# Optimization experiments

Hardware: AMD Instinct MI355X
Metric: run time of the kernel (lower is better)

## Reference

```python
import jax, jax.numpy as jnp
import numpy as np

L, B, S, D = 8, 1, 4096, 2048
H, KVH, HD = 16, 2, 128
Q = 32
THETA = 1e6
MROPE = (16, 24, 24)  # mrope_section, sums to HD//2
EPS = 1e-6


def setup_inputs() -> dict:
    key = jax.random.key(0)
    ks = jax.random.split(key, 8)
    hidden_states = jax.random.normal(ks[0], (L, B, S, D), dtype=jnp.float32)
    ln_w = jax.random.uniform(ks[1], (L, D), dtype=jnp.float32, minval=0.5, maxval=1.5)
    q_w = jax.random.normal(ks[2], (L, D, H * HD), dtype=jnp.float32) * 0.02
    q_b = jax.random.normal(ks[3], (L, H * HD), dtype=jnp.float32) * 0.02
    k_w = jax.random.normal(ks[4], (L, D, KVH * HD), dtype=jnp.float32) * 0.02
    k_b = jax.random.normal(ks[5], (L, KVH * HD), dtype=jnp.float32) * 0.02
    position_ids = jax.random.randint(ks[6], (3, B, S), 0, S, dtype=jnp.int32)
    q_idx = jnp.sort(jax.random.randint(ks[7], (Q,), 0, S, dtype=jnp.int32))
    return {"hidden_states": hidden_states, "ln_w": ln_w, "q_w": q_w, "q_b": q_b,
            "k_w": k_w, "k_b": k_b, "position_ids": position_ids, "q_idx": q_idx}


def _rot_half(x):
    h = x.shape[-1] // 2
    return jnp.concatenate([-x[..., h:], x[..., :h]], axis=-1)


def _mrope_combine(t):
    # t: (3, B, S, HD). Split last dim per 2*mrope_section, chunk i taken from axis i%3.
    parts, off = [], 0
    for i, sec in enumerate(MROPE):
        w = 2 * sec
        parts.append(t[i % 3, :, :, off:off + w])
        off += w
    return jnp.concatenate(parts, axis=-1)[:, None, :, :]  # (B, 1, S, HD)


def reference(hidden_states, ln_w, q_w, q_b, k_w, k_b, position_ids, q_idx):
    # Rotary embeddings from 3D mRoPE position ids
    inv_freq = 1.0 / (THETA ** (jnp.arange(0, HD, 2, dtype=jnp.float32) / HD))  # (HD/2,)
    freqs = position_ids.astype(jnp.float32)[..., None] * inv_freq  # (3, B, S, HD/2)
    emb = jnp.concatenate([freqs, freqs], axis=-1)  # (3, B, S, HD)
    cos = _mrope_combine(jnp.cos(emb))  # (B, 1, S, HD)
    sin = _mrope_combine(jnp.sin(emb))
    cos_q = cos[:, :, q_idx, :]  # (B, 1, Q, HD)
    sin_q = sin[:, :, q_idx, :]
    # Eager causal mask sliced at query rows: (Q, S)
    mask_add = jnp.where(jnp.arange(S)[None, :] > q_idx[:, None], -1e9, 0.0).astype(jnp.float32)

    scale = 1.0 / np.sqrt(HD).astype(np.float32)

    def per_layer(hs, lw, qw, qb, kw, kb):
        # RMSNorm (input_layernorm)
        var = jnp.mean(jnp.square(hs), axis=-1, keepdims=True)
        x = hs * jax.lax.rsqrt(var + EPS) * lw  # (B, S, D)
        xq = x[:, q_idx, :]  # (B, Q, D)
        k = (jnp.einsum('bsd,de->bse', x, kw) + kb).reshape(B, S, KVH, HD).transpose(0, 2, 1, 3)
        q = (jnp.einsum('bqd,de->bqe', xq, qw) + qb).reshape(B, Q, H, HD).transpose(0, 2, 1, 3)
        k = jnp.repeat(k, H // KVH, axis=1)  # repeat_kv -> (B, H, S, HD)
        k = k * cos + _rot_half(k) * sin
        q = q * cos_q + _rot_half(q) * sin_q
        scores = jnp.einsum('bhqd,bhkd->bhqk', q, k) * scale  # (B, H, Q, S)
        scores = scores + mask_add[None, None]
        return jax.nn.softmax(scores.astype(jnp.float32), axis=-1)

    return jax.vmap(per_layer)(hidden_states, ln_w, q_w, q_b, k_w, k_b)  # (L, B, H, Q, S)
```

## Files before the change

### kernel.cpp

```cpp
#include <hip/hip_runtime.h>
#include <hip/hip_bf16.h>
#include <math.h>

#define LYR 8
#define SEQ 4096
#define DIM 2048
#define NH 16
#define HD 128
#define NQ 32
#define NKV 256
#define NQE 2048

typedef __attribute__((ext_vector_type(8))) short short8;
typedef __attribute__((ext_vector_type(4))) float f32x4;

#define WS_IRQ   0
#define WS_ABLOB 256
#define WS_COS   524544
#define WS_SIN   1048832
#define WS_QBUF  1573120
#define WS_PART  2097408
#define WS_W2    4194560
#define WS_KBLOB 8388864
#define WS_QBLOB 16777472

__device__ __forceinline__ short f2bf(float x) {
  __hip_bfloat16 h = __float2bfloat16(x);
  return *(short*)&h;
}
__device__ __forceinline__ float bf2f(short s) {
  unsigned u = ((unsigned)(unsigned short)s) << 16;
  return __uint_as_float(u);
}

#define GLOAD16(srcp, dstp) \
  __builtin_amdgcn_global_load_lds( \
      (const __attribute__((address_space(1))) unsigned int*)(srcp), \
      (__attribute__((address_space(3))) unsigned int*)(dstp), 16, 0, 0)

#define RBAR() asm volatile("s_waitcnt lgkmcnt(0)\n\ts_barrier" ::: "memory")

__global__ __launch_bounds__(256) void prep_kernel(
    const float* __restrict__ ln_w, const float* __restrict__ k_w,
    short* __restrict__ W2) {
  int kb = blockIdx.x, l = blockIdx.y, t = threadIdx.x;
  const float* kwl = k_w + (size_t)l * DIM * NKV;
  const float* lnl = ln_w + l * DIM;
  short* blob = W2 + (size_t)(l * 64 + kb) * 16384;
  #pragma unroll
  for (int i = 0; i < 4; ++i) {
    int p = t + i * 256;
    int fi = p >> 6, lane = p & 63;
    int n = fi * 16 + (lane & 15);
    int k0 = kb * 32 + (lane >> 4) * 8;
    short hi8[8], lo8[8];
    #pragma unroll
    for (int e = 0; e < 8; ++e) {
      float v = lnl[k0 + e] * kwl[(size_t)(k0 + e) * NKV + n];
      short h = f2bf(v);
      hi8[e] = h;
      lo8[e] = f2bf(v - bf2f(h));
    }
    *(short8*)(blob + p * 8) = *(short8*)hi8;
    *(short8*)(blob + 8192 + p * 8) = *(short8*)lo8;
  }
}

__global__ __launch_bounds__(256) void rmsq_kernel(const float* __restrict__ hs,
                                                   const int* __restrict__ q_idx,
                                                   float* __restrict__ irq) {
  int qi = blockIdx.x, l = blockIdx.y, t = threadIdx.x;
  int s = q_idx[qi];
  const float* row = hs + ((size_t)l * SEQ + s) * DIM;
  float4 v0 = *(const float4*)(row + t * 4);
  float4 v1 = *(const float4*)(row + t * 4 + 1024);
  float acc = v0.x*v0.x + v0.y*v0.y + v0.z*v0.z + v0.w*v0.w
            + v1.x*v1.x + v1.y*v1.y + v1.z*v1.z + v1.w*v1.w;
  #pragma unroll
  for (int off = 32; off >= 1; off >>= 1) acc += __shfl_down(acc, off);
  __shared__ float red[4];
  if ((t & 63) == 0) red[t >> 6] = acc;
  __syncthreads();
  if (t == 0) {
    float tot = red[0] + red[1] + red[2] + red[3];
    irq[l * NQ + qi] = rsqrtf(tot / (float)DIM + 1e-6f);
  }
}

__global__ void cossin_kernel(const int* __restrict__ pos_ids,
                              float* __restrict__ cost, float* __restrict__ sint) {
  int idx = blockIdx.x * 256 + threadIdx.x;
  int s = idx >> 7, d = idx & 127;
  int t = (d < 32) ? 0 : (d < 80 ? 1 : 2);
  int j = d & 63;
  double invf = pow(1000000.0, -(double)j / 64.0);
  double ph = (double)pos_ids[t * SEQ + s] * invf;
  cost[idx] = (float)cos(ph);
  sint[idx] = (float)sin(ph);
}

__global__ __launch_bounds__(256) void xqt_kernel(
    const float* __restrict__ hs, const float* __restrict__ ln_w,
    const int* __restrict__ q_idx, const float* __restrict__ irq,
    short* __restrict__ Ablob) {
  __shared__ int qix[32];
  __shared__ float qir[32];
  int l = blockIdx.x, t = threadIdx.x;
  if (t < 32) { qix[t] = q_idx[t]; qir[t] = irq[l * NQ + t]; }
  __syncthreads();
  int lane = t & 63, g4 = t >> 6;
  short* base = Ablob + (size_t)l * 131072;
  int row = lane & 15, kgl = lane >> 4;
  for (int i = 0; i < 64; ++i) {
    int group = g4 * 64 + i;
    int kb = group >> 2, half = (group >> 1) & 1, mf = group & 1;
    int r = row + mf * 16;
    int k0 = kb * 32 + kgl * 8;
    const float* src = hs + ((size_t)l * SEQ + qix[r]) * DIM + k0;
    const float* lnp = ln_w + l * DIM + k0;
    float ir = qir[r];
    float4 v0 = *(const float4*)src;
    float4 v1 = *(const float4*)(src + 4);
    float4 w0 = *(const float4*)lnp;
    float4 w1 = *(const float4*)(lnp + 4);
    float av[8] = {v0.x*w0.x, v0.y*w0.y, v0.z*w0.z, v0.w*w0.w,
                   v1.x*w1.x, v1.y*w1.y, v1.z*w1.z, v1.w*w1.w};
    short o8[8];
    #pragma unroll
    for (int e = 0; e < 8; ++e) {
      float v = av[e] * ir;
      short h = f2bf(v);
      o8[e] = half ? f2bf(v - bf2f(h)) : h;
    }
    *(short8*)(base + group * 512 + lane * 8) = *(short8*)o8;
  }
}

__global__ __launch_bounds__(256) void kgemm_kernel(
    const float* __restrict__ hs, const short* __restrict__ W2,
    const float* __restrict__ k_b, const float* __restrict__ cost,
    const float* __restrict__ sint, short* __restrict__ Kblob) {
  __shared__ __align__(1024) char SM[67072];

  int t = threadIdx.x;
  int fid = blockIdx.x;
  int l = fid & 7, sb = fid >> 3;
  int s0 = sb * 64;
  int lane = t & 63, w = t >> 6;
  int fr = lane & 15, kg = lane >> 4;
  int arow = t >> 2, akg = t & 3;

  const float* hrow = hs + ((size_t)l * SEQ + s0 + arow) * DIM + akg * 8;
  const char* wbase = (const char*)(W2 + (size_t)l * 64 * 16384);
  const char* wfrag = wbase + w * 1024 + lane * 16;

  int amf = arow >> 4;
  int awoff = amf * 1024 + (((akg * 16 + (arow & 15)) * 16) ^ (akg << 5));
  int aroff = (lane * 16) ^ ((lane >> 4) << 5);

  f32x4 acc[4][4];
  #pragma unroll
  for (int mf = 0; mf < 4; ++mf)
    #pragma unroll
    for (int nf = 0; nf < 4; ++nf) acc[mf][nf] = (f32x4){0.f, 0.f, 0.f, 0.f};
  float sq = 0.f;
  float4 rA0, rA1, rB0, rB1;
  short8 B0h[4], B0l[4], B1h[4], B1l[4];

  {
    #pragma unroll
    for (int nf = 0; nf < 4; ++nf) {
      B0h[nf] = *(const short8*)(wfrag + nf * 4096);
      B0l[nf] = *(const short8*)(wfrag + nf * 4096 + 16384);
    }
    float4 a0 = *(const float4*)(hrow);
    float4 a1 = *(const float4*)(hrow + 4);
    float av[8] = {a0.x, a0.y, a0.z, a0.w, a1.x, a1.y, a1.z, a1.w};
    short hi8[8], lo8[8];
    #pragma unroll
    for (int e = 0; e < 8; ++e) {
      sq += av[e] * av[e];
      short h = f2bf(av[e]);
      hi8[e] = h;
      lo8[e] = f2bf(av[e] - bf2f(h));
    }
    *(short8*)(SM + awoff) = *(short8*)hi8;
    *(short8*)(SM + 4096 + awoff) = *(short8*)lo8;
    rA0 = *(const float4*)(hrow + 32);
    rA1 = *(const float4*)(hrow + 36);
  }
  RBAR();

#define KSTEP(KB, CA0, CA1, NA0, NA1, UBH, UBL, PBH, PBL) do { \
    int buf_ = (KB) & 1; \
    char* asb_ = SM + buf_ * 8192; \
    if ((KB) < 63) { \
      const char* bsrc_ = wfrag + (size_t)((KB) + 1) * 32768; \
      _Pragma("unroll") \
      for (int nf = 0; nf < 4; ++nf) { \
        PBH[nf] = *(const short8*)(bsrc_ + nf * 4096); \
        PBL[nf] = *(const short8*)(bsrc_ + nf * 4096 + 16384); \
      } \
    } \
    if ((KB) < 62) { \
      NA0 = *(const float4*)(hrow + ((KB) + 2) * 32); \
      NA1 = *(const float4*)(hrow + ((KB) + 2) * 32 + 4); \
    } \
    short8 ah_[4], al_[4]; \
    _Pragma("unroll") \
    for (int mf = 0; mf < 4; ++mf) { \
      ah_[mf] = *(const short8*)(asb_ + mf * 1024 + aroff); \
      al_[mf] = *(const short8*)(asb_ + 4096 + mf * 1024 + aroff); \
    } \
    __builtin_amdgcn_s_setprio(1); \
    _Pragma("unroll") \
    for (int nf = 0; nf < 4; ++nf) { \
      _Pragma("unroll") \
      for (int mf = 0; mf < 4; ++mf) { \
        acc[mf][nf] = __builtin_amdgcn_mfma_f32_16x16x32_bf16(ah_[mf], UBH[nf], acc[mf][nf], 0, 0, 0); \
        acc[mf][nf] = __builtin_amdgcn_mfma_f32_16x16x32_bf16(ah_[mf], UBL[nf], acc[mf][nf], 0, 0, 0); \
        acc[mf][nf] = __builtin_amdgcn_mfma_f32_16x16x32_bf16(al_[mf], UBH[nf], acc[mf][nf], 0, 0, 0); \
      } \
    } \
    __builtin_amdgcn_s_setprio(0); \
    if ((KB) < 63) { \
      char* asn_ = SM + (buf_ ^ 1) * 8192; \
      float av_[8] = {CA0.x, CA0.y, CA0.z, CA0.w, CA1.x, CA1.y, CA1.z, CA1.w}; \
      short hi8_[8], lo8_[8]; \
      _Pragma("unroll") \
      for (int e = 0; e < 8; ++e) { \
        sq += av_[e] * av_[e]; \
        short h_ = f2bf(av_[e]); \
        hi8_[e] = h_; \
        lo8_[e] = f2bf(av_[e] - bf2f(h_)); \
      } \
      *(short8*)(asn_ + awoff) = *(short8*)hi8_; \
      *(short8*)(asn_ + 4096 + awoff) = *(short8*)lo8_; \
    } \
    RBAR(); \
  } while (0)

  for (int kb2 = 0; kb2 < 32; ++kb2) {
    KSTEP(2 * kb2,     rA0, rA1, rB0, rB1, B0h, B0l, B1h, B1l);
    KSTEP(2 * kb2 + 1, rB0, rB1, rA0, rA1, B1h, B1l, B0h, B0l);
  }
#undef KSTEP

  sq += __shfl_xor(sq, 1);
  sq += __shfl_xor(sq, 2);
  float* irs = (float*)(SM + 66560);
  if ((t & 3) == 0) irs[arow] = rsqrtf(sq / (float)DIM + 1e-6f);
  __syncthreads();

  float* Kraw = (float*)SM;
  int j = w * 16 + fr;
  float bias0 = k_b[l * NKV + j];
  float bias1 = k_b[l * NKV + j + 64];
  float bias2 = k_b[l * NKV + j + 128];
  float bias3 = k_b[l * NKV + j + 192];
  #pragma unroll
  for (int mf = 0; mf < 4; ++mf) {
    #pragma unroll
    for (int r = 0; r < 4; ++r) {
      int row = mf * 16 + kg * 4 + r;
      int s = s0 + row;
      float ir = irs[row];
      float v0 = acc[mf][0][r] * ir + bias0;
      float v1 = acc[mf][1][r] * ir + bias1;
      float v2 = acc[mf][2][r] * ir + bias2;
      float v3 = acc[mf][3][r] * ir + bias3;
      float cj = cost[s * HD + j], sj = sint[s * HD + j];
      float cj2 = cost[s * HD + j + 64], sj2 = sint[s * HD + j + 64];
      float* kr = Kraw + row * 260;
      kr[j]       = v0 * cj - v1 * sj;
      kr[j + 64]  = v1 * cj2 + v0 * sj2;
      kr[j + 128] = v2 * cj - v3 * sj;
      kr[j + 192] = v3 * cj2 + v2 * sj2;
    }
  }
  __syncthreads();

  int kc = sb >> 1, fb = (sb & 1) * 4;
  #pragma unroll
  for (int i = 0; i < 8; ++i) {
    int c = t + i * 256;
    int lc = c & 63, fl = (c >> 6) & 3, ts = (c >> 8) & 3, kv = c >> 10;
    int key = fl * 16 + (lc & 15);
    int d0 = kv * 128 + ts * 32 + (lc >> 4) * 8;
    float4 x0 = *(const float4*)(Kraw + key * 260 + d0);
    float4 x1 = *(const float4*)(Kraw + key * 260 + d0 + 4);
    float av[8] = {x0.x, x0.y, x0.z, x0.w, x1.x, x1.y, x1.z, x1.w};
    short hi8[8], lo8[8];
    #pragma unroll
    for (int e = 0; e < 8; ++e) {
      short h = f2bf(av[e]);
      hi8[e] = h;
      lo8[e] = f2bf(av[e] - bf2f(h));
    }
    short* bb = Kblob + (size_t)((l * 2 + kv) * 32 + kc) * 32768
              + (size_t)((ts * 2 + 0) * 8 + fb + fl) * 512 + lc * 8;
    *(short8*)bb = *(short8*)hi8;
    *(short8*)(bb + 4096) = *(short8*)lo8;
  }
}

__global__ __launch_bounds__(512) void qgemm_kernel(
    const float* __restrict__ q_w, const short* __restrict__ Ablob,
    float* __restrict__ part) {
  __shared__ __align__(1024) char SM[131072];
  int t = threadIdx.x;
  int nc = blockIdx.x, ks = blockIdx.y, l = blockIdx.z;
  int lane = t & 63, w = t >> 6;
  int fr = lane & 15, kg = lane >> 4;
  const char* abase = (const char*)(Ablob + (size_t)l * 131072 + (size_t)ks * 32768);
  const float* qwl = q_w + (size_t)l * DIM * NQE;

  #pragma unroll
  for (int c = 0; c < 8; ++c) {
    int chunk = w * 8 + c;
    GLOAD16(abase + chunk * 1024 + lane * 16, SM + chunk * 1024);
  }
  #pragma unroll
  for (int c = 0; c < 4; ++c) {
    int r = w * 4 + c;
    GLOAD16((const char*)(qwl + (size_t)(ks * 512 + r) * NQE + nc * 256) + lane * 16,
            SM + 65536 + r * 1024 + lane * 16);
  }
  f32x4 acc[2][2];
  #pragma unroll
  for (int mf = 0; mf < 2; ++mf)
    #pragma unroll
    for (int nf = 0; nf < 2; ++nf) acc[mf][nf] = (f32x4){0.f, 0.f, 0.f, 0.f};
  __syncthreads();

  for (int ts = 0; ts < 16; ++ts) {
    int buf = ts & 1;
    if (ts < 15) {
      #pragma unroll
      for (int c = 0; c < 4; ++c) {
        int r = w * 4 + c;
        GLOAD16((const char*)(qwl + (size_t)(ks * 512 + (ts + 1) * 32 + r) * NQE + nc * 256) + lane * 16,
                SM + 65536 + (buf ^ 1) * 32768 + r * 1024 + lane * 16);
      }
    }
    short8 ah[2], al[2];
    #pragma unroll
    for (int mf = 0; mf < 2; ++mf) {
      ah[mf] = *(const short8*)(SM + ts * 4096 + mf * 1024 + lane * 16);
      al[mf] = *(const short8*)(SM + ts * 4096 + 2048 + mf * 1024 + lane * 16);
    }
    const float* bt = (const float*)(SM + 65536 + buf * 32768);
    #pragma unroll
    for (int nf = 0; nf < 2; ++nf) {
      int c = w * 32 + nf * 16 + fr;
      short bh8[8], bl8[8];
      #pragma unroll
      for (int e = 0; e < 8; ++e) {
        float v = bt[(kg * 8 + e) * 256 + c];
        short h = f2bf(v);
        bh8[e] = h;
        bl8[e] = f2bf(v - bf2f(h));
      }
      short8 bh = *(short8*)bh8, bl = *(short8*)bl8;
      #pragma unroll
      for (int mf = 0; mf < 2; ++mf) {
        acc[mf][nf] = __builtin_amdgcn_mfma_f32_16x16x32_bf16(ah[mf], bh, acc[mf][nf], 0, 0, 0);
        acc[mf][nf] = __builtin_amdgcn_mfma_f32_16x16x32_bf16(ah[mf], bl, acc[mf][nf], 0, 0, 0);
        acc[mf][nf] = __builtin_amdgcn_mfma_f32_16x16x32_bf16(al[mf], bh, acc[mf][nf], 0, 0, 0);
      }
    }
    __syncthreads();
  }

  #pragma unroll
  for (int mf = 0; mf < 2; ++mf) {
    #pragma unroll
    for (int r = 0; r < 4; ++r) {
      int row = mf * 16 + kg * 4 + r;
      float* prow = part + ((size_t)((ks * LYR + l) * NQ + row)) * NQE + nc * 256;
      #pragma unroll
      for (int nf = 0; nf < 2; ++nf) {
        int col = w * 32 + nf * 16 + fr;
        prow[col] = acc[mf][nf][r];
      }
    }
  }
}

__global__ __launch_bounds__(256) void qred_kernel(
    const float* __restrict__ part, const float* __restrict__ q_b,
    float* __restrict__ Qbuf) {
  int idx = blockIdx.x * 256 + threadIdx.x;
  int n = idx & 2047, q = (idx >> 11) & 31, l = idx >> 16;
  float v = q_b[l * NQE + n];
  #pragma unroll
  for (int ks = 0; ks < 4; ++ks)
    v += part[((size_t)((ks * LYR + l) * NQ + q)) * NQE + n];
  Qbuf[((size_t)l * NQ + q) * NQE + n] = v;
}

__global__ __launch_bounds__(256) void qpack_kernel(
    const float* __restrict__ Qbuf, const float* __restrict__ cost,
    const float* __restrict__ sint, const int* __restrict__ q_idx,
    short* __restrict__ Qblob) {
  int kv = blockIdx.x, l = blockIdx.y, t = threadIdx.x;
  short* blob = Qblob + (size_t)(l * 2 + kv) * 65536;
  #pragma unroll
  for (int i = 0; i < 16; ++i) {
    int p = t + i * 256;
    int ts = p >> 10, f = (p >> 6) & 15, lane = p & 63;
    int row = f * 16 + (lane & 15);
    int hh = row >> 5, q = row & 31;
    int h = kv * 8 + hh;
    int d0 = ts * 32 + (lane >> 4) * 8;
    int s = q_idx[q];
    const float* qrow = Qbuf + ((size_t)l * NQ + q) * NQE + h * HD;
    const float* ct = cost + s * HD;
    const float* st = sint + s * HD;
    short hi8[8], lo8[8];
    #pragma unroll
    for (int e = 0; e < 8; ++e) {
      int d = d0 + e;
      float x = qrow[d];
      float xp = qrow[d ^ 64];
      float v = (d < 64) ? (x * ct[d] - xp * st[d]) : (x * ct[d] + xp * st[d]);
      short h2 = f2bf(v);
      hi8[e] = h2;
      lo8[e] = f2bf(v - bf2f(h2));
    }
    *(short8*)(blob + ((ts * 2 + 0) * 16 + f) * 512 + lane * 8) = *(short8*)hi8;
    *(short8*)(blob + ((ts * 2 + 1) * 16 + f) * 512 + lane * 8) = *(short8*)lo8;
  }
}

__global__ __launch_bounds__(512) void scores_kernel(
    const short* __restrict__ Qblob, const short* __restrict__ Kblob,
    const int* __restrict__ q_idx, float* __restrict__ out) {
  __shared__ short Qs[2][16384];
  __shared__ short Ks[2][8192];
  __shared__ int qiv[32];
  int t = threadIdx.x;
  int kc = blockIdx.x, kv = blockIdx.y, l = blockIdx.z;
  int lane = t & 63, w = t >> 6;
  int wm = w >> 1, wn = w & 1;
  if (t < 32) qiv[t] = q_idx[t];
  const char* qsrc = (const char*)(Qblob + (size_t)(l * 2 + kv) * 65536);
  const char* ksrc = (const char*)(Kblob + (size_t)((l * 2 + kv) * 32 + kc) * 32768);
  #pragma unroll
  for (int c = 0; c < 4; ++c) {
    int off = (w * 4 + c) * 1024;
    GLOAD16(qsrc + off + lane * 16, (char*)Qs[0] + off);
  }
  #pragma unroll
  for (int c = 0; c < 2; ++c) {
    int off = (w * 2 + c) * 1024;
    GLOAD16(ksrc + off + lane * 16, (char*)Ks[0] + off);
  }
  f32x4 acc[4][4];
  #pragma unroll
  for (int mf = 0; mf < 4; ++mf)
    #pragma unroll
    for (int nf = 0; nf < 4; ++nf) acc[mf][nf] = (f32x4){0.f, 0.f, 0.f, 0.f};
  __syncthreads();
  for (int ts = 0; ts < 4; ++ts) {
    int buf = ts & 1;
    if (ts < 3) {
      const char* qs = qsrc + (ts + 1) * 32768;
      const char* ks = ksrc + (ts + 1) * 16384;
      #pragma unroll
      for (int c = 0; c < 4; ++c) {
        int off = (w * 4 + c) * 1024;
        GLOAD16(qs + off + lane * 16, (char*)Qs[(ts + 1) & 1] + off);
      }
      #pragma unroll
      for (int c = 0; c < 2; ++c) {
        int off = (w * 2 + c) * 1024;
        GLOAD16(ks + off + lane * 16, (char*)Ks[(ts + 1) & 1] + off);
      }
    }
    short8 ah[4], al[4];
    #pragma unroll
    for (int mf = 0; mf < 4; ++mf) {
      int f = wm * 4 + mf;
      ah[mf] = *(const short8*)(Qs[buf] + f * 512 + lane * 8);
      al[mf] = *(const short8*)(Qs[buf] + 8192 + f * 512 + lane * 8);
    }
    #pragma unroll
    for (int nf = 0; nf < 4; ++nf) {
      int f = wn * 4 + nf;
      short8 bh = *(const short8*)(Ks[buf] + f * 512 + lane * 8);
      short8 bl = *(const short8*)(Ks[buf] + 4096 + f * 512 + lane * 8);
      #pragma unroll
      for (int mf = 0; mf < 4; ++mf) {
        acc[mf][nf] = __builtin_amdgcn_mfma_f32_16x16x32_bf16(ah[mf], bh, acc[mf][nf], 0, 0, 0);
        acc[mf][nf] = __builtin_amdgcn_mfma_f32_16x16x32_bf16(ah[mf], bl, acc[mf][nf], 0, 0, 0);
        acc[mf][nf] = __builtin_amdgcn_mfma_f32_16x16x32_bf16(al[mf], bh, acc[mf][nf], 0, 0, 0);
      }
    }
    __syncthreads();
  }
  const float scale = 0.088388347648318447f;
  #pragma unroll
  for (int mf = 0; mf < 4; ++mf) {
    #pragma unroll
    for (int r = 0; r < 4; ++r) {
      int rr = wm * 64 + mf * 16 + (lane >> 4) * 4 + r;
      int hh = rr >> 5, q = rr & 31;
      int qv = qiv[q];
      float* orow = out + (((size_t)(l * NH + kv * 8 + hh)) * NQ + q) * SEQ;
      #pragma unroll
      for (int nf = 0; nf < 4; ++nf) {
        int key = kc * 128 + (wn * 4 + nf) * 16 + (lane & 15);
        orow[key] = (key > qv) ? -1e9f : acc[mf][nf][r] * scale;
      }
    }
  }
}

__global__ __launch_bounds__(256) void softmax_kernel(float* __restrict__ out) {
  size_t row = blockIdx.x;
  float* p = out + row * SEQ;
  int t = threadIdx.x;
  float4 v[4];
  float mx = -1e30f;
  #pragma unroll
  for (int i = 0; i < 4; ++i) {
    v[i] = *(const float4*)(p + t * 4 + i * 1024);
    mx = fmaxf(mx, fmaxf(fmaxf(v[i].x, v[i].y), fmaxf(v[i].z, v[i].w)));
  }
  #pragma unroll
  for (int off = 32; off >= 1; off >>= 1) mx = fmaxf(mx, __shfl_xor(mx, off));
  __shared__ float red[4];
  if ((t & 63) == 0) red[t >> 6] = mx;
  __syncthreads();
  mx = fmaxf(fmaxf(red[0], red[1]), fmaxf(red[2], red[3]));
  __syncthreads();
  float sum = 0.f;
  #pragma unroll
  for (int i = 0; i < 4; ++i) {
    v[i].x = __expf(v[i].x - mx); v[i].y = __expf(v[i].y - mx);
    v[i].z = __expf(v[i].z - mx); v[i].w = __expf(v[i].w - mx);
    sum += v[i].x + v[i].y + v[i].z + v[i].w;
  }
  #pragma unroll
  for (int off = 32; off >= 1; off >>= 1) sum += __shfl_xor(sum, off);
  if ((t & 63) == 0) red[t >> 6] = sum;
  __syncthreads();
  sum = red[0] + red[1] + red[2] + red[3];
  float inv = 1.f / sum;
  #pragma unroll
  for (int i = 0; i < 4; ++i) {
    v[i].x *= inv; v[i].y *= inv; v[i].z *= inv; v[i].w *= inv;
    *(float4*)(p + t * 4 + i * 1024) = v[i];
  }
}

extern "C" void kernel_launch(void* const* d_in, const int* in_sizes, int n_in,
                              void* d_out, int out_size, void* d_ws, size_t ws_size,
                              hipStream_t stream) {
  const float* hs   = (const float*)d_in[0];
  const float* ln_w = (const float*)d_in[1];
  const float* q_w  = (const float*)d_in[2];
  const float* q_b  = (const float*)d_in[3];
  const float* k_w  = (const float*)d_in[4];
  const float* k_b  = (const float*)d_in[5];
  const int* pos    = (const int*)d_in[6];
  const int* qidx   = (const int*)d_in[7];
  float* out = (float*)d_out;
  float* ws = (float*)d_ws;
  float* irq   = ws + WS_IRQ;
  short* Ablob = (short*)(ws + WS_ABLOB);
  float* cost  = ws + WS_COS;
  float* sint  = ws + WS_SIN;
  float* Qbuf  = ws + WS_QBUF;
  float* part  = ws + WS_PART;
  short* W2    = (short*)(ws + WS_W2);
  short* Kblob = (short*)(ws + WS_KBLOB);
  short* Qblob = (short*)(ws + WS_QBLOB);

  prep_kernel<<<dim3(64, LYR), 256, 0, stream>>>(ln_w, k_w, W2);
  rmsq_kernel<<<dim3(NQ, LYR), 256, 0, stream>>>(hs, qidx, irq);
  cossin_kernel<<<(SEQ * HD) / 256, 256, 0, stream>>>(pos, cost, sint);
  xqt_kernel<<<LYR, 256, 0, stream>>>(hs, ln_w, qidx, irq, Ablob);
  kgemm_kernel<<<512, 256, 0, stream>>>(hs, W2, k_b, cost, sint, Kblob);
  qgemm_kernel<<<dim3(8, 4, LYR), 512, 0, stream>>>(q_w, Ablob, part);
  qred_kernel<<<2048, 256, 0, stream>>>(part, q_b, Qbuf);
  qpack_kernel<<<dim3(2, LYR), 256, 0, stream>>>(Qbuf, cost, sint, qidx, Qblob);
  scores_kernel<<<dim3(32, 2, LYR), 512, 0, stream>>>(Qblob, Kblob, qidx, out);
  softmax_kernel<<<LYR * NH * NQ, 256, 0, stream>>>(out);
}
```

Baseline: 279.8 us.

## Split-bf16 via bit truncation, interleave MFMA halves with LDS staging, swizzle K tile

```diff
diff --git a/kernel.cpp b/kernel.cpp
--- a/kernel.cpp
+++ b/kernel.cpp
@@ -31,6 +31,13 @@
 __device__ __forceinline__ float bf2f(short s) {
   unsigned u = ((unsigned)(unsigned short)s) << 16;
   return __uint_as_float(u);
+}
+
+__device__ __forceinline__ void split1(float x, short& h, short& l) {
+  unsigned b = __float_as_uint(x);
+  h = (short)(b >> 16);
+  float lo = x - __uint_as_float(b & 0xffff0000u);
+  l = (short)((__float_as_uint(lo) + 0x8000u) >> 16);
 }
 
 #define GLOAD16(srcp, dstp) \
@@ -129,8 +136,9 @@
     #pragma unroll
     for (int e = 0; e < 8; ++e) {
       float v = av[e] * ir;
-      short h = f2bf(v);
-      o8[e] = half ? f2bf(v - bf2f(h)) : h;
+      short hh, ll;
+      split1(v, hh, ll);
+      o8[e] = half ? ll : hh;
     }
     *(short8*)(base + group * 512 + lane * 8) = *(short8*)o8;
   }
@@ -140,7 +148,7 @@
     const float* __restrict__ hs, const short* __restrict__ W2,
     const float* __restrict__ k_b, const float* __restrict__ cost,
     const float* __restrict__ sint, short* __restrict__ Kblob) {
-  __shared__ __align__(1024) char SM[67072];
+  __shared__ __align__(1024) char SM[65536];
 
   int t = threadIdx.x;
   int fid = blockIdx.x;
@@ -154,8 +162,7 @@
   const char* wbase = (const char*)(W2 + (size_t)l * 64 * 16384);
   const char* wfrag = wbase + w * 1024 + lane * 16;
 
-  int amf = arow >> 4;
-  int awoff = amf * 1024 + (((akg * 16 + (arow & 15)) * 16) ^ (akg << 5));
+  int awoff = (arow >> 4) * 1024 + (((akg * 16 + (arow & 15)) * 16) ^ (akg << 5));
   int aroff = (lane * 16) ^ ((lane >> 4) << 5);
 
   f32x4 acc[4][4];
@@ -179,10 +186,8 @@
     short hi8[8], lo8[8];
     #pragma unroll
     for (int e = 0; e < 8; ++e) {
-      sq += av[e] * av[e];
-      short h = f2bf(av[e]);
-      hi8[e] = h;
-      lo8[e] = f2bf(av[e] - bf2f(h));
+      sq = fmaf(av[e], av[e], sq);
+      split1(av[e], hi8[e], lo8[e]);
     }
     *(short8*)(SM + awoff) = *(short8*)hi8;
     *(short8*)(SM + 4096 + awoff) = *(short8*)lo8;
@@ -191,9 +196,10 @@
   }
   RBAR();
 
-#define KSTEP(KB, CA0, CA1, NA0, NA1, UBH, UBL, PBH, PBL) do { \
+#define KSTEP8(KB, CA0, CA1, NA0, NA1, UBH, UBL, PBH, PBL) do { \
     int buf_ = (KB) & 1; \
-    char* asb_ = SM + buf_ * 8192; \
+    const char* asb_ = SM + buf_ * 8192; \
+     \
     if ((KB) < 63) { \
       const char* bsrc_ = wfrag + (size_t)((KB) + 1) * 32768; \
       _Pragma("unroll") \
@@ -212,47 +218,81 @@
       ah_[mf] = *(const short8*)(asb_ + mf * 1024 + aroff); \
       al_[mf] = *(const short8*)(asb_ + 4096 + mf * 1024 + aroff); \
     } \
+    __builtin_amdgcn_s_barrier(); \
+    asm volatile("s_waitcnt lgkmcnt(0)" ::: "memory"); \
     __builtin_amdgcn_s_setprio(1); \
     _Pragma("unroll") \
-    for (int nf = 0; nf < 4; ++nf) { \
-      _Pragma("unroll") \
-      for (int mf = 0; mf < 4; ++mf) { \
+    for (int nf = 0; nf < 2; ++nf) \
+      _Pragma("unroll") \
+      for (int mf = 0; mf < 4; ++mf) \
         acc[mf][nf] = __builtin_amdgcn_mfma_f32_16x16x32_bf16(ah_[mf], UBH[nf], acc[mf][nf], 0, 0, 0); \
+    _Pragma("unroll") \
+    for (int nf = 0; nf < 2; ++nf) \
+      _Pragma("unroll") \
+      for (int mf = 0; mf < 4; ++mf) \
         acc[mf][nf] = __builtin_amdgcn_mfma_f32_16x16x32_bf16(ah_[mf], UBL[nf], acc[mf][nf], 0, 0, 0); \
+    _Pragma("unroll") \
+    for (int nf = 0; nf < 2; ++nf) \
+      _Pragma("unroll") \
+      for (int mf = 0; mf < 4; ++mf) \
         acc[mf][nf] = __builtin_amdgcn_mfma_f32_16x16x32_bf16(al_[mf], UBH[nf], acc[mf][nf], 0, 0, 0); \
-      } \
-    } \
     __builtin_amdgcn_s_setprio(0); \
+    __builtin_amdgcn_s_barrier(); \
+     \
     if ((KB) < 63) { \
       char* asn_ = SM + (buf_ ^ 1) * 8192; \
       float av_[8] = {CA0.x, CA0.y, CA0.z, CA0.w, CA1.x, CA1.y, CA1.z, CA1.w}; \
       short hi8_[8], lo8_[8]; \
       _Pragma("unroll") \
       for (int e = 0; e < 8; ++e) { \
-        sq += av_[e] * av_[e]; \
-        short h_ = f2bf(av_[e]); \
-        hi8_[e] = h_; \
-        lo8_[e] = f2bf(av_[e] - bf2f(h_)); \
+        sq = fmaf(av_[e], av_[e], sq); \
+        split1(av_[e], hi8_[e], lo8_[e]); \
       } \
       *(short8*)(asn_ + awoff) = *(short8*)hi8_; \
       *(short8*)(asn_ + 4096 + awoff) = *(short8*)lo8_; \
     } \
-    RBAR(); \
+    __builtin_amdgcn_s_setprio(1); \
+    _Pragma("unroll") \
+    for (int nf = 2; nf < 4; ++nf) \
+      _Pragma("unroll") \
+      for (int mf = 0; mf < 4; ++mf) \
+        acc[mf][nf] = __builtin_amdgcn_mfma_f32_16x16x32_bf16(ah_[mf], UBH[nf], acc[mf][nf], 0, 0, 0); \
+    _Pragma("unroll") \
+    for (int nf = 2; nf < 4; ++nf) \
+      _Pragma("unroll") \
+      for (int mf = 0; mf < 4; ++mf) \
+        acc[mf][nf] = __builtin_amdgcn_mfma_f32_16x16x32_bf16(ah_[mf], UBL[nf], acc[mf][nf], 0, 0, 0); \
+    _Pragma("unroll") \
+    for (int nf = 2; nf < 4; ++nf) \
+      _Pragma("unroll") \
+      for (int mf = 0; mf < 4; ++mf) \
+        acc[mf][nf] = __builtin_amdgcn_mfma_f32_16x16x32_bf16(al_[mf], UBH[nf], acc[mf][nf], 0, 0, 0); \
+    __builtin_amdgcn_s_setprio(0); \
+    asm volatile("s_waitcnt lgkmcnt(0)" ::: "memory"); \
+    __builtin_amdgcn_s_barrier(); \
   } while (0)
 
   for (int kb2 = 0; kb2 < 32; ++kb2) {
-    KSTEP(2 * kb2,     rA0, rA1, rB0, rB1, B0h, B0l, B1h, B1l);
-    KSTEP(2 * kb2 + 1, rB0, rB1, rA0, rA1, B1h, B1l, B0h, B0l);
-  }
-#undef KSTEP
+    KSTEP8(2 * kb2,     rA0, rA1, rB0, rB1, B0h, B0l, B1h, B1l);
+    KSTEP8(2 * kb2 + 1, rB0, rB1, rA0, rA1, B1h, B1l, B0h, B0l);
+  }
+#undef KSTEP8
 
   sq += __shfl_xor(sq, 1);
   sq += __shfl_xor(sq, 2);
-  float* irs = (float*)(SM + 66560);
-  if ((t & 3) == 0) irs[arow] = rsqrtf(sq / (float)DIM + 1e-6f);
-  __syncthreads();
-
-  float* Kraw = (float*)SM;
+  float* smf = (float*)SM;
+  __syncthreads();
+  if ((t & 3) == 0) smf[arow] = sq;
+  __syncthreads();
+  float irv[16];
+  #pragma unroll
+  for (int mf = 0; mf < 4; ++mf)
+    #pragma unroll
+    for (int r = 0; r < 4; ++r)
+      irv[mf * 4 + r] = rsqrtf(smf[mf * 16 + kg * 4 + r] / (float)DIM + 1e-6f);
+  __syncthreads();
+
+  float* Kraw = smf;
   int j = w * 16 + fr;
   float bias0 = k_b[l * NKV + j];
   float bias1 = k_b[l * NKV + j + 64];
@@ -264,18 +304,19 @@
     for (int r = 0; r < 4; ++r) {
       int row = mf * 16 + kg * 4 + r;
       int s = s0 + row;
-      float ir = irs[row];
+      float ir = irv[mf * 4 + r];
       float v0 = acc[mf][0][r] * ir + bias0;
       float v1 = acc[mf][1][r] * ir + bias1;
       float v2 = acc[mf][2][r] * ir + bias2;
       float v3 = acc[mf][3][r] * ir + bias3;
       float cj = cost[s * HD + j], sj = sint[s * HD + j];
       float cj2 = cost[s * HD + j + 64], sj2 = sint[s * HD + j + 64];
-      float* kr = Kraw + row * 260;
-      kr[j]       = v0 * cj - v1 * sj;
-      kr[j + 64]  = v1 * cj2 + v0 * sj2;
-      kr[j + 128] = v2 * cj - v3 * sj;
-      kr[j + 192] = v3 * cj2 + v2 * sj2;
+      int sw = (row & 7) << 2;
+      float* kr = Kraw + row * 256;
+      kr[j ^ sw]           = v0 * cj - v1 * sj;
+      kr[(j + 64) ^ sw]    = v1 * cj2 + v0 * sj2;
+      kr[(j + 128) ^ sw]   = v2 * cj - v3 * sj;
+      kr[(j + 192) ^ sw]   = v3 * cj2 + v2 * sj2;
     }
   }
   __syncthreads();
@@ -284,21 +325,18 @@
   #pragma unroll
   for (int i = 0; i < 8; ++i) {
     int c = t + i * 256;
-    int lc = c & 63, fl = (c >> 6) & 3, ts = (c >> 8) & 3, kv = c >> 10;
+    int lc = c & 63, fl = (c >> 6) & 3, ts2 = (c >> 8) & 3, kv = c >> 10;
     int key = fl * 16 + (lc & 15);
-    int d0 = kv * 128 + ts * 32 + (lc >> 4) * 8;
-    float4 x0 = *(const float4*)(Kraw + key * 260 + d0);
-    float4 x1 = *(const float4*)(Kraw + key * 260 + d0 + 4);
+    int d0 = kv * 128 + ts2 * 32 + (lc >> 4) * 8;
+    int sw = (key & 7) << 2;
+    float4 x0 = *(const float4*)(Kraw + key * 256 + (d0 ^ sw));
+    float4 x1 = *(const float4*)(Kraw + key * 256 + ((d0 + 4) ^ sw));
     float av[8] = {x0.x, x0.y, x0.z, x0.w, x1.x, x1.y, x1.z, x1.w};
     short hi8[8], lo8[8];
     #pragma unroll
-    for (int e = 0; e < 8; ++e) {
-      short h = f2bf(av[e]);
-      hi8[e] = h;
-      lo8[e] = f2bf(av[e] - bf2f(h));
-    }
+    for (int e = 0; e < 8; ++e) split1(av[e], hi8[e], lo8[e]);
     short* bb = Kblob + (size_t)((l * 2 + kv) * 32 + kc) * 32768
-              + (size_t)((ts * 2 + 0) * 8 + fb + fl) * 512 + lc * 8;
+              + (size_t)((ts2 * 2 + 0) * 8 + fb + fl) * 512 + lc * 8;
     *(short8*)bb = *(short8*)hi8;
     *(short8*)(bb + 4096) = *(short8*)lo8;
   }
@@ -350,6 +388,7 @@
       al[mf] = *(const short8*)(SM + ts * 4096 + 2048 + mf * 1024 + lane * 16);
     }
     const float* bt = (const float*)(SM + 65536 + buf * 32768);
+    short8 bh[2], bl[2];
     #pragma unroll
     for (int nf = 0; nf < 2; ++nf) {
       int c = w * 32 + nf * 16 + fr;
@@ -357,18 +396,26 @@
       #pragma unroll
       for (int e = 0; e < 8; ++e) {
         float v = bt[(kg * 8 + e) * 256 + c];
-        short h = f2bf(v);
-        bh8[e] = h;
-        bl8[e] = f2bf(v - bf2f(h));
+        split1(v, bh8[e], bl8[e]);
       }
-      short8 bh = *(short8*)bh8, bl = *(short8*)bl8;
-      #pragma unroll
-      for (int mf = 0; mf < 2; ++mf) {
-        acc[mf][nf] = __builtin_amdgcn_mfma_f32_16x16x32_bf16(ah[mf], bh, acc[mf][nf], 0, 0, 0);
-        acc[mf][nf] = __builtin_amdgcn_mfma_f32_16x16x32_bf16(ah[mf], bl, acc[mf][nf], 0, 0, 0);
-        acc[mf][nf] = __builtin_amdgcn_mfma_f32_16x16x32_bf16(al[mf], bh, acc[mf][nf], 0, 0, 0);
-      }
-    }
+      bh[nf] = *(short8*)bh8;
+      bl[nf] = *(short8*)bl8;
+    }
+    #pragma unroll
+    for (int nf = 0; nf < 2; ++nf)
+      #pragma unroll
+      for (int mf = 0; mf < 2; ++mf)
+        acc[mf][nf] = __builtin_amdgcn_mfma_f32_16x16x32_bf16(ah[mf], bh[nf], acc[mf][nf], 0, 0, 0);
+    #pragma unroll
+    for (int nf = 0; nf < 2; ++nf)
+      #pragma unroll
+      for (int mf = 0; mf < 2; ++mf)
+        acc[mf][nf] = __builtin_amdgcn_mfma_f32_16x16x32_bf16(ah[mf], bl[nf], acc[mf][nf], 0, 0, 0);
+    #pragma unroll
+    for (int nf = 0; nf < 2; ++nf)
+      #pragma unroll
+      for (int mf = 0; mf < 2; ++mf)
+        acc[mf][nf] = __builtin_amdgcn_mfma_f32_16x16x32_bf16(al[mf], bh[nf], acc[mf][nf], 0, 0, 0);
     __syncthreads();
   }
 
@@ -424,9 +471,7 @@
       float x = qrow[d];
       float xp = qrow[d ^ 64];
       float v = (d < 64) ? (x * ct[d] - xp * st[d]) : (x * ct[d] + xp * st[d]);
-      short h2 = f2bf(v);
-      hi8[e] = h2;
-      lo8[e] = f2bf(v - bf2f(h2));
+      split1(v, hi8[e], lo8[e]);
     }
     *(short8*)(blob + ((ts * 2 + 0) * 16 + f) * 512 + lane * 8) = *(short8*)hi8;
     *(short8*)(blob + ((ts * 2 + 1) * 16 + f) * 512 + lane * 8) = *(short8*)lo8;
@@ -485,18 +530,28 @@
       ah[mf] = *(const short8*)(Qs[buf] + f * 512 + lane * 8);
       al[mf] = *(const short8*)(Qs[buf] + 8192 + f * 512 + lane * 8);
     }
+    short8 bh[4], bl[4];
     #pragma unroll
     for (int nf = 0; nf < 4; ++nf) {
       int f = wn * 4 + nf;
-      short8 bh = *(const short8*)(Ks[buf] + f * 512 + lane * 8);
-      short8 bl = *(const short8*)(Ks[buf] + 4096 + f * 512 + lane * 8);
-      #pragma unroll
-      for (int mf = 0; mf < 4; ++mf) {
-        acc[mf][nf] = __builtin_amdgcn_mfma_f32_16x16x32_bf16(ah[mf], bh, acc[mf][nf], 0, 0, 0);
-        acc[mf][nf] = __builtin_amdgcn_mfma_f32_16x16x32_bf16(ah[mf], bl, acc[mf][nf], 0, 0, 0);
-        acc[mf][nf] = __builtin_amdgcn_mfma_f32_16x16x32_bf16(al[mf], bh, acc[mf][nf], 0, 0, 0);
-      }
-    }
+      bh[nf] = *(const short8*)(Ks[buf] + f * 512 + lane * 8);
+      bl[nf] = *(const short8*)(Ks[buf] + 4096 + f * 512 + lane * 8);
+    }
+    #pragma unroll
+    for (int nf = 0; nf < 4; ++nf)
+      #pragma unroll
+      for (int mf = 0; mf < 4; ++mf)
+        acc[mf][nf] = __builtin_amdgcn_mfma_f32_16x16x32_bf16(ah[mf], bh[nf], acc[mf][nf], 0, 0, 0);
+    #pragma unroll
+    for (int nf = 0; nf < 4; ++nf)
+      #pragma unroll
+      for (int mf = 0; mf < 4; ++mf)
+        acc[mf][nf] = __builtin_amdgcn_mfma_f32_16x16x32_bf16(ah[mf], bl[nf], acc[mf][nf], 0, 0, 0);
+    #pragma unroll
+    for (int nf = 0; nf < 4; ++nf)
+      #pragma unroll
+      for (int mf = 0; mf < 4; ++mf)
+        acc[mf][nf] = __builtin_amdgcn_mfma_f32_16x16x32_bf16(al[mf], bh[nf], acc[mf][nf], 0, 0, 0);
     __syncthreads();
   }
   const float scale = 0.088388347648318447f;
```

Measured after the change: 267.0 us. -4.6%, faster.
